# Kernel optimization log

Measured on AMD Instinct MI355X. Metric: run time of the kernel, lower is better.

The kernel has to match this reference:

```python
import jax, jax.numpy as jnp
import numpy as np

EPS = 1e-5

def _bin_act(x):
    # sign() forward, clipped straight-through estimator backward
    xc = jnp.clip(x, -1.0, 1.0)
    return xc + jax.lax.stop_gradient(jnp.sign(x) - xc)

def _bin_w(w):
    # XNOR-style: sign(w) scaled by per-output-channel mean(|w|); identity STE
    alpha = jnp.mean(jnp.abs(w), axis=(1, 2, 3), keepdims=True)
    return w + jax.lax.stop_gradient(jnp.sign(w) * alpha - w)

def _conv(x, w, stride, padding, groups):
    return jax.lax.conv_general_dilated(
        x, w, window_strides=(stride, stride),
        padding=[(padding, padding), (padding, padding)],
        feature_group_count=groups,
        dimension_numbers=('NCHW', 'OIHW', 'NCHW'))

def _binconv(x, w, stride, padding, groups):
    return _conv(_bin_act(x), _bin_w(w), stride, padding, groups)

def _bn(x, g, b, m, v):
    # eval-mode BatchNorm2d
    inv = g / jnp.sqrt(v + EPS)
    return x * inv[None, :, None, None] + (b - m * inv)[None, :, None, None]


def setup_inputs() -> dict:
    key = jax.random.key(0)
    ks = jax.random.split(key, 20)
    inp, oup = 256, 512
    d = {}
    d['x'] = jax.random.normal(ks[0], (64, inp, 28, 28), jnp.float32)
    d['w1'] = jax.random.normal(ks[1], (inp, 16, 3, 3), jnp.float32) * 0.1  # grouped, groups=inp/16
    d['w2'] = jax.random.normal(ks[2], (oup, inp, 1, 1), jnp.float32) * 0.05
    d['w3'] = jax.random.normal(ks[3], (oup, oup, 1, 1), jnp.float32) * 0.05
    for i, (name, c) in enumerate([('1', inp), ('2', oup), ('3', oup)]):
        d['g' + name] = jax.random.uniform(ks[4 + 4 * i], (c,), jnp.float32, 0.5, 1.5)
        d['b' + name] = jax.random.normal(ks[5 + 4 * i], (c,), jnp.float32) * 0.1
        d['m' + name] = jax.random.normal(ks[6 + 4 * i], (c,), jnp.float32) * 0.1
        d['v' + name] = jax.random.uniform(ks[7 + 4 * i], (c,), jnp.float32, 0.5, 1.5)
    return d


def reference(x, w1, w2, w3, g1, b1, m1, v1, g2, b2, m2, v2, g3, b3, m3, v3):
    inp = x.shape[1]
    groups = inp // 16
    # conv1 (binary grouped 3x3) + bn1 + residual + hardtanh
    out = _bn(_binconv(x, w1, 1, 1, groups), g1, b1, m1, v1)
    out = jnp.clip(out + x, -1.0, 1.0)
    # conv2 (binary 1x1, inp->oup) + bn2 + hardtanh
    out = jnp.clip(_bn(_binconv(out, w2, 1, 0, 1), g2, b2, m2, v2), -1.0, 1.0)
    res = out
    # conv3 (binary 1x1, oup->oup) + bn3 + residual + hardtanh
    out = _bn(_binconv(out, w3, 1, 0, 1), g3, b3, m3, v3)
    return jnp.clip(out + res, -1.0, 1.0)
```

## Files before the change

kernel.cpp:

```cpp
#include <hip/hip_runtime.h>
#include <stdint.h>

#define C1 256
#define C2 512
#define P_ 784
#define TAU 1e-6
#define PT 56


__global__ __launch_bounds__(256) void prep(
    const float* __restrict__ w1, const float* __restrict__ w2, const float* __restrict__ w3,
    const float* __restrict__ g1, const float* __restrict__ b1, const float* __restrict__ m1, const float* __restrict__ v1,
    const float* __restrict__ g2, const float* __restrict__ b2, const float* __restrict__ m2, const float* __restrict__ v2,
    const float* __restrict__ g3, const float* __restrict__ b3, const float* __restrict__ m3, const float* __restrict__ v3,
    double* __restrict__ sc1d, double* __restrict__ bi1d,
    int* __restrict__ T2, float* __restrict__ sc2f, float* __restrict__ bi2f,
    float* __restrict__ sc3f, float* __restrict__ bi3f,
    uint16_t* __restrict__ wb1, uint32_t* __restrict__ bw2, uint32_t* __restrict__ bw3,
    unsigned long long* __restrict__ amin)
{
    int bid = blockIdx.x, t = threadIdx.x;
    if (bid == 0 && t == 0) amin[0] = ~0ULL;
    if (bid == 0) {
        int co = t;
        const float* wp = w1 + (size_t)co * 144;
        double s = 0.0;
        for (int k = 0; k < 144; k++) s += fabs((double)wp[k]);
        double alpha = s / 144.0;
        double iv = (double)g1[co] / sqrt((double)v1[co] + 1e-5);
        sc1d[co] = alpha * iv;
        bi1d[co] = (double)b1[co] - (double)m1[co] * iv;
        for (int tap = 0; tap < 9; tap++) {
            uint32_t wv = 0;
            for (int ci = 0; ci < 16; ci++) wv |= (uint32_t)(wp[ci * 9 + tap] < 0.f) << ci;
            wb1[co * 9 + tap] = (uint16_t)wv;
        }
    } else if (bid <= 2) {
        int co = (bid - 1) * 256 + t;
        const float* wp = w2 + (size_t)co * 256;
        double s = 0.0;
        for (int k = 0; k < 256; k++) s += fabs((double)wp[k]);
        double alpha = s / 256.0;
        double iv = (double)g2[co] / sqrt((double)v2[co] + 1e-5);
        double sc = alpha * iv;
        double bi = (double)b2[co] - (double)m2[co] * iv;
        int T = -257;
        while (T <= 257 && fma((double)T, sc, bi) < 0.0) T++;
        T2[co] = T;
        sc2f[co] = (float)sc;
        bi2f[co] = (float)bi;
        for (int wd = 0; wd < 8; wd++) {
            uint32_t wv = 0;
            for (int j = 0; j < 32; j++) wv |= (uint32_t)(wp[wd * 32 + j] < 0.f) << j;
            bw2[co * 8 + wd] = wv;
        }
    } else {
        int co = (bid - 3) * 256 + t;
        const float* wp = w3 + (size_t)co * 512;
        double s = 0.0;
        for (int k = 0; k < 512; k++) s += fabs((double)wp[k]);
        double alpha = s / 512.0;
        double iv = (double)g3[co] / sqrt((double)v3[co] + 1e-5);
        sc3f[co] = (float)(alpha * iv);
        bi3f[co] = (float)((double)b3[co] - (double)m3[co] * iv);
        for (int wd = 0; wd < 16; wd++) {
            uint32_t wv = 0;
            for (int j = 0; j < 32; j++) wv |= (uint32_t)(wp[wd * 32 + j] < 0.f) << j;
            bw3[co * 16 + wd] = wv;
        }
    }
}

__global__ __launch_bounds__(256) void k1(
    const float* __restrict__ x,
    const double* __restrict__ sc1d, const double* __restrict__ bi1d,
    const uint16_t* __restrict__ wb1,
    uint16_t* __restrict__ pk1, unsigned long long* __restrict__ amin)
{
    __shared__ uint32_t xzb[30][30];
    __shared__ uint16_t wbl[16][9];
    __shared__ double scs[16], bis[16];

    int g = blockIdx.x, n = blockIdx.y, t = threadIdx.x;

    for (int idx = t; idx < 900; idx += 256) ((uint32_t*)xzb)[idx] = 0;
    if (t < 144) ((uint16_t*)wbl)[t] = wb1[g * 144 + t];
    if (t < 16) { scs[t] = sc1d[g * 16 + t]; bis[t] = bi1d[g * 16 + t]; }
    __syncthreads();

    const float* xg = x + ((size_t)n * C1 + g * 16) * P_;
    float xr[4][16];
    #pragma unroll
    for (int i = 0; i < 4; i++) {
        int p = t + 256 * i;
        if (p < P_) {
            uint32_t sb = 0, nb = 0;
            #pragma unroll
            for (int ci = 0; ci < 16; ci++) {
                float xv = xg[ci * P_ + p];
                xr[i][ci] = xv;
                sb |= (uint32_t)(xv < 0.f) << ci;
                nb |= (uint32_t)(xv != 0.f) << ci;
            }
            int h = p / 28, w = p - 28 * h;
            xzb[h + 1][w + 1] = sb | (nb << 16);
        }
    }
    __syncthreads();

    uint16_t* pko = pk1 + (size_t)n * P_ * 16;
    #pragma unroll
    for (int i = 0; i < 4; i++) {
        int p = t + 256 * i;
        if (p < P_) {
            int h = p / 28, w = p - 28 * h;
            uint32_t xv9[9], zv9[9];
            int Z = 0;
            #pragma unroll
            for (int kh = 0; kh < 3; kh++)
                #pragma unroll
                for (int kw = 0; kw < 3; kw++) {
                    int k = kh * 3 + kw;
                    uint32_t xz = xzb[h + kh][w + kw];
                    xv9[k] = xz & 0xFFFFu;
                    zv9[k] = xz >> 16;
                    Z += __popc(zv9[k]);
                }
            uint32_t word = 0;
            #pragma unroll
            for (int co = 0; co < 16; co++) {
                int pd = 0;
                #pragma unroll
                for (int k = 0; k < 9; k++)
                    pd += __popc((xv9[k] ^ (uint32_t)wbl[co][k]) & zv9[k]);
                int S = Z - 2 * pd;
                double v = fma((double)S, scs[co], bis[co]) + (double)xr[i][co];
                v = fmin(fmax(v, -1.0), 1.0);
                double m = fabs(v);
                if (m < TAU) {
                    unsigned long long pk =
                        ((unsigned long long)__float_as_uint((float)m) << 32) |
                        (unsigned long long)((uint32_t)(n * C1 + g * 16 + co) * (uint32_t)P_ + (uint32_t)p);
                    atomicMin(amin, pk);
                }
                word |= (uint32_t)(v < 0.0) << co;
            }
            pko[(size_t)p * 16 + g] = (uint16_t)word;
        }
    }
}

__global__ __launch_bounds__(512) void k23(
    const uint32_t* __restrict__ bw2, const uint32_t* __restrict__ bw3,
    const int* __restrict__ T2, const float* __restrict__ sc2f, const float* __restrict__ bi2f,
    const float* __restrict__ sc3f, const float* __restrict__ bi3f,
    const uint16_t* __restrict__ pk1, const unsigned long long* __restrict__ amin,
    float* __restrict__ out)
{
    __shared__ uint32_t xw2[PT][8];
    __shared__ uint32_t xw3[PT][16];

    int pc = blockIdx.x, n = blockIdx.y, t = threadIdx.x;
    int p0 = pc * PT;
    int wv = t >> 6, lane = t & 63;

    const uint32_t* pkw = (const uint32_t*)(pk1 + (size_t)n * P_ * 16);
    for (int idx = t; idx < PT * 8; idx += 512)
        ((uint32_t*)xw2)[idx] = pkw[(size_t)p0 * 8 + idx];
    __syncthreads();
    if (t == 0) {
        unsigned long long a = amin[0];
        if (a != ~0ULL) {
            uint32_t loc = (uint32_t)a;
            uint32_t nn = loc / (C1 * P_);
            uint32_t rem = loc - nn * C1 * P_;
            uint32_t c = rem / P_, p = rem - c * P_;
            if ((int)nn == n && (int)p >= p0 && (int)p < p0 + PT)
                xw2[p - p0][c >> 5] ^= 1u << (c & 31);
        }
    }
    __syncthreads();

    int co = t;
    float r2f[PT];
    {
        const uint32_t* wp = bw2 + co * 8;
        uint32_t w0 = wp[0], w1 = wp[1], w2 = wp[2], w3 = wp[3];
        uint32_t w4 = wp[4], w5 = wp[5], w6 = wp[6], w7 = wp[7];
        int Tv = T2[co];
        float scf = sc2f[co], bif = bi2f[co];
        #pragma unroll
        for (int p = 0; p < PT; p++) {
            const uint32_t* xp = xw2[p];
            int pop = __popc(xp[0] ^ w0) + __popc(xp[1] ^ w1) + __popc(xp[2] ^ w2) + __popc(xp[3] ^ w3)
                    + __popc(xp[4] ^ w4) + __popc(xp[5] ^ w5) + __popc(xp[6] ^ w6) + __popc(xp[7] ^ w7);
            int S = 256 - 2 * pop;
            float vf = __fmaf_rn((float)S, scf, bif);
            r2f[p] = fminf(fmaxf(vf, -1.f), 1.f);
            unsigned long long mb = __ballot(S < Tv);
            if (lane == 0) {
                xw3[p][2 * wv]     = (uint32_t)mb;
                xw3[p][2 * wv + 1] = (uint32_t)(mb >> 32);
            }
        }
    }
    __syncthreads();

    {
        const uint32_t* wp = bw3 + co * 16;
        uint32_t w[16];
        #pragma unroll
        for (int i = 0; i < 16; i++) w[i] = wp[i];
        float sc = sc3f[co], bi = bi3f[co];
        float* op = out + ((size_t)n * C2 + co) * P_ + p0;
        float4 b4;
        #pragma unroll
        for (int p = 0; p < PT; p++) {
            const uint32_t* xp = xw3[p];
            int pop = 0;
            #pragma unroll
            for (int i = 0; i < 16; i++) pop += __popc(xp[i] ^ w[i]);
            int S = 512 - 2 * pop;
            float v = __fmaf_rn((float)S, sc, bi) + r2f[p];
            v = fminf(fmaxf(v, -1.f), 1.f);
            int r = p & 3;
            if (r == 0) b4.x = v; else if (r == 1) b4.y = v; else if (r == 2) b4.z = v;
            else { b4.w = v; ((float4*)op)[p >> 2] = b4; }
        }
    }
}

extern "C" void kernel_launch(void* const* d_in, const int* in_sizes, int n_in,
                              void* d_out, int out_size, void* d_ws, size_t ws_size,
                              hipStream_t stream) {
    const float* x  = (const float*)d_in[0];
    const float* w1 = (const float*)d_in[1];
    const float* w2 = (const float*)d_in[2];
    const float* w3 = (const float*)d_in[3];
    const float* g1 = (const float*)d_in[4];
    const float* b1 = (const float*)d_in[5];
    const float* m1 = (const float*)d_in[6];
    const float* v1 = (const float*)d_in[7];
    const float* g2 = (const float*)d_in[8];
    const float* b2 = (const float*)d_in[9];
    const float* m2 = (const float*)d_in[10];
    const float* v2 = (const float*)d_in[11];
    const float* g3 = (const float*)d_in[12];
    const float* b3 = (const float*)d_in[13];
    const float* m3 = (const float*)d_in[14];
    const float* v3 = (const float*)d_in[15];
    float* out = (float*)d_out;

    char* ws = (char*)d_ws;
    unsigned long long* amin = (unsigned long long*)(ws + 0);
    double*   sc1d = (double*)(ws + 64);
    double*   bi1d = (double*)(ws + 2112);
    int*      T2   = (int*)(ws + 4160);
    float*    sc2f = (float*)(ws + 6208);
    float*    bi2f = (float*)(ws + 8256);
    float*    sc3f = (float*)(ws + 10304);
    float*    bi3f = (float*)(ws + 12352);
    uint16_t* wb1  = (uint16_t*)(ws + 14400);
    uint32_t* bw2  = (uint32_t*)(ws + 19008);
    uint32_t* bw3  = (uint32_t*)(ws + 35392);
    uint16_t* pk1  = (uint16_t*)(ws + 68160);

    prep<<<dim3(5), 256, 0, stream>>>(w1, w2, w3,
        g1, b1, m1, v1, g2, b2, m2, v2, g3, b3, m3, v3,
        sc1d, bi1d, T2, sc2f, bi2f, sc3f, bi3f, wb1, bw2, bw3, amin);
    k1<<<dim3(16, 64), 256, 0, stream>>>(x, sc1d, bi1d, wb1, pk1, amin);
    k23<<<dim3(P_ / PT, 64), 512, 0, stream>>>(bw2, bw3, T2, sc2f, bi2f, sc3f, bi3f, pk1, amin, out);
}
```

Measured before the change: 133.2 us.

## Use float fast path in k1, group-major pk1 layout, chunked k23 with smaller register footprint

k1 now computes the BN+residual value in float and falls back to the double-precision path and atomic tie-tracking only when the value is near zero. k1 writes its packed sign words in a group-major layout so each thread's store is contiguous across p; k23 then transposes them through shared memory. k23 processes positions in chunks of 8 with double-buffered ballot words, which removes the 56-float r2f register array and should raise occupancy. The grid order is also swapped. This adds a shared-memory transpose stage and one barrier per chunk in exchange for fewer registers and coalesced stores.

```diff
diff --git a/kernel.cpp b/kernel.cpp
--- a/kernel.cpp
+++ b/kernel.cpp
@@ -6,6 +6,7 @@
 #define P_ 784
 #define TAU 1e-6
 #define PT 56
+#define CH 8
 
 
 __global__ __launch_bounds__(256) void prep(
@@ -80,12 +81,16 @@
     __shared__ uint32_t xzb[30][30];
     __shared__ uint16_t wbl[16][9];
     __shared__ double scs[16], bis[16];
+    __shared__ float scf[16], bif[16];
 
     int g = blockIdx.x, n = blockIdx.y, t = threadIdx.x;
 
     for (int idx = t; idx < 900; idx += 256) ((uint32_t*)xzb)[idx] = 0;
     if (t < 144) ((uint16_t*)wbl)[t] = wb1[g * 144 + t];
-    if (t < 16) { scs[t] = sc1d[g * 16 + t]; bis[t] = bi1d[g * 16 + t]; }
+    if (t < 16) {
+        scs[t] = sc1d[g * 16 + t]; bis[t] = bi1d[g * 16 + t];
+        scf[t] = (float)scs[t];    bif[t] = (float)bis[t];
+    }
     __syncthreads();
 
     const float* xg = x + ((size_t)n * C1 + g * 16) * P_;
@@ -108,7 +113,7 @@
     }
     __syncthreads();
 
-    uint16_t* pko = pk1 + (size_t)n * P_ * 16;
+    uint16_t* pko = pk1 + ((size_t)n * 16 + g) * P_;
     #pragma unroll
     for (int i = 0; i < 4; i++) {
         int p = t + 256 * i;
@@ -134,18 +139,25 @@
                 for (int k = 0; k < 9; k++)
                     pd += __popc((xv9[k] ^ (uint32_t)wbl[co][k]) & zv9[k]);
                 int S = Z - 2 * pd;
-                double v = fma((double)S, scs[co], bis[co]) + (double)xr[i][co];
-                v = fmin(fmax(v, -1.0), 1.0);
-                double m = fabs(v);
-                if (m < TAU) {
-                    unsigned long long pk =
-                        ((unsigned long long)__float_as_uint((float)m) << 32) |
-                        (unsigned long long)((uint32_t)(n * C1 + g * 16 + co) * (uint32_t)P_ + (uint32_t)p);
-                    atomicMin(amin, pk);
+                float vf = __fmaf_rn((float)S, scf[co], bif[co]) + xr[i][co];
+                uint32_t neg;
+                if (fabsf(vf) < 1e-3f) {
+                    double v = fma((double)S, scs[co], bis[co]) + (double)xr[i][co];
+                    v = fmin(fmax(v, -1.0), 1.0);
+                    double m = fabs(v);
+                    if (m < TAU) {
+                        unsigned long long pk =
+                            ((unsigned long long)__float_as_uint((float)m) << 32) |
+                            (unsigned long long)((uint32_t)(n * C1 + g * 16 + co) * (uint32_t)P_ + (uint32_t)p);
+                        atomicMin(amin, pk);
+                    }
+                    neg = (v < 0.0);
+                } else {
+                    neg = (vf < 0.f);
                 }
-                word |= (uint32_t)(v < 0.0) << co;
+                word |= neg << co;
             }
-            pko[(size_t)p * 16 + g] = (uint16_t)word;
+            pko[p] = (uint16_t)word;
         }
     }
 }
@@ -157,16 +169,19 @@
     const uint16_t* __restrict__ pk1, const unsigned long long* __restrict__ amin,
     float* __restrict__ out)
 {
+    __shared__ uint16_t raw[16][PT];
     __shared__ uint32_t xw2[PT][8];
-    __shared__ uint32_t xw3[PT][16];
-
-    int pc = blockIdx.x, n = blockIdx.y, t = threadIdx.x;
+    __shared__ uint32_t xw3[2][CH][16];
+
+    int n = blockIdx.x, pc = blockIdx.y, t = threadIdx.x;
     int p0 = pc * PT;
     int wv = t >> 6, lane = t & 63;
 
-    const uint32_t* pkw = (const uint32_t*)(pk1 + (size_t)n * P_ * 16);
-    for (int idx = t; idx < PT * 8; idx += 512)
-        ((uint32_t*)xw2)[idx] = pkw[(size_t)p0 * 8 + idx];
+    const uint32_t* pkw = (const uint32_t*)(pk1 + (size_t)n * 16 * P_);
+    for (int idx = t; idx < 16 * (PT / 2); idx += 512) {
+        int g = idx / (PT / 2), j = idx % (PT / 2);
+        ((uint32_t*)raw)[g * (PT / 2) + j] = pkw[g * (P_ / 2) + p0 / 2 + j];
+    }
     __syncthreads();
     if (t == 0) {
         unsigned long long a = amin[0];
@@ -176,56 +191,60 @@
             uint32_t rem = loc - nn * C1 * P_;
             uint32_t c = rem / P_, p = rem - c * P_;
             if ((int)nn == n && (int)p >= p0 && (int)p < p0 + PT)
-                xw2[p - p0][c >> 5] ^= 1u << (c & 31);
-        }
+                raw[c >> 4][p - p0] ^= (uint16_t)(1u << (c & 15));
+        }
+    }
+    __syncthreads();
+    for (int idx = t; idx < PT * 8; idx += 512) {
+        int p = idx >> 3, wd = idx & 7;
+        xw2[p][wd] = (uint32_t)raw[2 * wd][p] | ((uint32_t)raw[2 * wd + 1][p] << 16);
     }
     __syncthreads();
 
     int co = t;
-    float r2f[PT];
-    {
-        const uint32_t* wp = bw2 + co * 8;
-        uint32_t w0 = wp[0], w1 = wp[1], w2 = wp[2], w3 = wp[3];
-        uint32_t w4 = wp[4], w5 = wp[5], w6 = wp[6], w7 = wp[7];
-        int Tv = T2[co];
-        float scf = sc2f[co], bif = bi2f[co];
+    const uint32_t* wp2 = bw2 + co * 8;
+    uint32_t a0 = wp2[0], a1 = wp2[1], a2 = wp2[2], a3 = wp2[3];
+    uint32_t a4 = wp2[4], a5 = wp2[5], a6 = wp2[6], a7 = wp2[7];
+    int Tv = T2[co];
+    float sc2 = sc2f[co], bi2v = bi2f[co];
+    const uint32_t* wp3 = bw3 + co * 16;
+    uint32_t w[16];
+    #pragma unroll
+    for (int i = 0; i < 16; i++) w[i] = wp3[i];
+    float sc3 = sc3f[co], bi3v = bi3f[co];
+    float* op = out + ((size_t)n * C2 + co) * P_ + p0;
+
+    for (int c = 0; c < PT / CH; c++) {
+        int buf = c & 1;
+        float r2[CH];
         #pragma unroll
-        for (int p = 0; p < PT; p++) {
-            const uint32_t* xp = xw2[p];
-            int pop = __popc(xp[0] ^ w0) + __popc(xp[1] ^ w1) + __popc(xp[2] ^ w2) + __popc(xp[3] ^ w3)
-                    + __popc(xp[4] ^ w4) + __popc(xp[5] ^ w5) + __popc(xp[6] ^ w6) + __popc(xp[7] ^ w7);
+        for (int j = 0; j < CH; j++) {
+            const uint32_t* xp = xw2[CH * c + j];
+            int pop = __popc(xp[0] ^ a0) + __popc(xp[1] ^ a1) + __popc(xp[2] ^ a2) + __popc(xp[3] ^ a3)
+                    + __popc(xp[4] ^ a4) + __popc(xp[5] ^ a5) + __popc(xp[6] ^ a6) + __popc(xp[7] ^ a7);
             int S = 256 - 2 * pop;
-            float vf = __fmaf_rn((float)S, scf, bif);
-            r2f[p] = fminf(fmaxf(vf, -1.f), 1.f);
+            float vf = __fmaf_rn((float)S, sc2, bi2v);
+            r2[j] = fminf(fmaxf(vf, -1.f), 1.f);
             unsigned long long mb = __ballot(S < Tv);
             if (lane == 0) {
-                xw3[p][2 * wv]     = (uint32_t)mb;
-                xw3[p][2 * wv + 1] = (uint32_t)(mb >> 32);
+                xw3[buf][j][2 * wv]     = (uint32_t)mb;
+                xw3[buf][j][2 * wv + 1] = (uint32_t)(mb >> 32);
             }
         }
-    }
-    __syncthreads();
-
-    {
-        const uint32_t* wp = bw3 + co * 16;
-        uint32_t w[16];
-        #pragma unroll
-        for (int i = 0; i < 16; i++) w[i] = wp[i];
-        float sc = sc3f[co], bi = bi3f[co];
-        float* op = out + ((size_t)n * C2 + co) * P_ + p0;
+        __syncthreads();
         float4 b4;
         #pragma unroll
-        for (int p = 0; p < PT; p++) {
-            const uint32_t* xp = xw3[p];
+        for (int j = 0; j < CH; j++) {
+            const uint32_t* xp = xw3[buf][j];
             int pop = 0;
             #pragma unroll
             for (int i = 0; i < 16; i++) pop += __popc(xp[i] ^ w[i]);
             int S = 512 - 2 * pop;
-            float v = __fmaf_rn((float)S, sc, bi) + r2f[p];
+            float v = __fmaf_rn((float)S, sc3, bi3v) + r2[j];
             v = fminf(fmaxf(v, -1.f), 1.f);
-            int r = p & 3;
+            int r = j & 3;
             if (r == 0) b4.x = v; else if (r == 1) b4.y = v; else if (r == 2) b4.z = v;
-            else { b4.w = v; ((float4*)op)[p >> 2] = b4; }
+            else { b4.w = v; ((float4*)op)[(CH * c + j) >> 2] = b4; }
         }
     }
 }
@@ -269,5 +288,5 @@
         g1, b1, m1, v1, g2, b2, m2, v2, g3, b3, m3, v3,
         sc1d, bi1d, T2, sc2f, bi2f, sc3f, bi3f, wb1, bw2, bw3, amin);
     k1<<<dim3(16, 64), 256, 0, stream>>>(x, sc1d, bi1d, wb1, pk1, amin);
-    k23<<<dim3(P_ / PT, 64), 512, 0, stream>>>(bw2, bw3, T2, sc2f, bi2f, sc3f, bi3f, pk1, amin, out);
-}
+    k23<<<dim3(64, P_ / PT), 512, 0, stream>>>(bw2, bw3, T2, sc2f, bi2f, sc3f, bi3f, pk1, amin, out);
+}
```

Result: no change. 131.3 us (-1.4%).
